# Kernel tuning notes

Hardware: AMD Instinct MI355X
Metric: run time of the kernel (lower is better)

The kernel has to match this reference:

```python
import jax, jax.numpy as jnp
import numpy as np

S, N, IN = 4096, 32, 4
H, IF, SF, OUT = 64, 8, 4, 2
N_PAIRS = N * (N - 1)


def setup_inputs() -> dict:
    key = jax.random.key(0)
    ks = jax.random.split(key, 12)
    f = jax.random.normal
    return {
        "inputs": f(ks[0], (S, N, IN), jnp.float32),
        "L1W": f(ks[1], (H, IN), jnp.float32) * 0.1,
        "L1b": f(ks[2], (H,), jnp.float32) * 0.1,
        "L2W": f(ks[3], (H, H), jnp.float32) * 0.1,
        "L2b": f(ks[4], (H,), jnp.float32) * 0.1,
        "I1W": f(ks[5], (H, H), jnp.float32) * 0.1,
        "I2W": f(ks[6], (IF, H), jnp.float32) * 0.1,
        "I3": f(ks[7], (N_PAIRS, OUT, IF // OUT), jnp.float32) * 0.01,
        "S1W": f(ks[8], (SF, IN), jnp.float32) * 0.1,
        "S1b": f(ks[9], (SF,), jnp.float32) * 0.1,
        "S2W": f(ks[10], (N, OUT, SF // OUT), jnp.float32) * 0.01,
        "S2b": jnp.zeros((N, OUT), jnp.float32),
    }


def reference(inputs, L1W, L1b, L2W, L2b, I1W, I2W, I3, S1W, S1b, S2W, S2b):
    seq_len, n_obj = inputs.shape[:2]
    out_size = S2b.shape[1]

    # shared encoders (torch Linear: x @ W.T + b)
    h = jax.nn.relu(inputs @ L1W.T + L1b)
    h = jax.nn.relu(h @ L2W.T + L2b)          # [S, N, H]
    hs = jax.nn.relu(inputs @ S1W.T + S1b)    # [S, N, SF]

    # all pairwise differences Xi - Xj -> edge MLP (no biases)
    diff = h[:, :, None, :] - h[:, None, :, :]      # [S, N, N, H]
    pair = jnp.tanh(diff @ I1W.T)                   # [S, N, N, H]
    pair = jnp.tanh(pair @ I2W.T)                   # [S, N, N, IF]
    k_int = pair.shape[-1] // out_size
    pair = pair.reshape(seq_len, n_obj, n_obj, out_size, k_int)

    # scatter per-pair weights I3 into dense [N, N, OUT, k] using the
    # row-major Table ordering (i, j != i); diagonal stays zero, which
    # matches the original since diag pairwise features are exactly 0.
    ii, jj = np.nonzero(~np.eye(n_obj, dtype=bool))
    I3d = jnp.zeros((n_obj, n_obj, out_size, k_int), I3.dtype).at[ii, jj].set(I3)

    interaction = jnp.einsum('sijdk,ijdk->sid', pair, I3d)  # [S, N, OUT]

    k_self = hs.shape[-1] // out_size
    hs = hs.reshape(seq_len, n_obj, out_size, k_self)
    self_term = jnp.einsum('sidk,idk->sid', hs, S2W) + S2b  # [S, N, OUT]

    return interaction + self_term
```

## Files before the change

kernel.cpp:

```cpp
#include <hip/hip_runtime.h>
#include <math.h>

#define SEQ   4096
#define NOBJ  32
#define IN_F  4
#define HID   64
#define IFEAT 8
#define NPAIR_HALF 496
#define NTILE 31

#define TWO_LOG2E 2.8853900817779268f

#if __has_builtin(__builtin_amdgcn_exp2f)
  #define EXP2F(x) __builtin_amdgcn_exp2f(x)
#else
  #define EXP2F(x) exp2f(x)
#endif

typedef _Float16 h2    __attribute__((ext_vector_type(2)));
typedef _Float16 f16x8 __attribute__((ext_vector_type(8)));
typedef float    f32x4 __attribute__((ext_vector_type(4)));

__device__ __forceinline__ h2 pack2(float a, float b) {
  return __builtin_bit_cast(h2, __builtin_amdgcn_cvt_pkrtz(a, b));
}
__device__ __forceinline__ unsigned pbits(h2 v) { return __builtin_bit_cast(unsigned, v); }

__device__ __forceinline__ f16x8 pack8(float4 a, float4 b) {
  int4 v;
  v.x = (int)pbits(pack2(a.x, a.y));
  v.y = (int)pbits(pack2(a.z, a.w));
  v.z = (int)pbits(pack2(b.x, b.y));
  v.w = (int)pbits(pack2(b.z, b.w));
  return __builtin_bit_cast(f16x8, v);
}

__device__ __forceinline__ f16x8 pack8f(const float* r) {
  int4 v;
  v.x = (int)pbits(pack2(r[0], r[1]));
  v.y = (int)pbits(pack2(r[2], r[3]));
  v.z = (int)pbits(pack2(r[4], r[5]));
  v.w = (int)pbits(pack2(r[6], r[7]));
  return __builtin_bit_cast(f16x8, v);
}

__device__ __forceinline__ float tanh_u(float x) {
  float e = EXP2F(x * TWO_LOG2E);
  float r = __builtin_amdgcn_rcpf(e + 1.0f);
  return fmaf(-2.0f, r, 1.0f);
}

__device__ __forceinline__ int pair_cum(int i) { return (i * (63 - i)) >> 1; }

__device__ __forceinline__ void pair_decode(int q, int& i, int& j) {
  int ii = (int)((63.0f - sqrtf(3969.0f - 8.0f * (float)q)) * 0.5f);
  if (ii > 0 && pair_cum(ii) > q) --ii;
  if (pair_cum(ii + 1) <= q)     ++ii;
  i = ii;
  j = ii + 1 + (q - pair_cum(ii));
}

__global__ __launch_bounds__(256, 4) void magnet_fused(
    const float* __restrict__ x,
    const float* __restrict__ L1W,
    const float* __restrict__ L1b,
    const float* __restrict__ L2W,
    const float* __restrict__ L2b,
    const float* __restrict__ I1W,
    const float* __restrict__ I2W,
    const float* __restrict__ I3,
    const float* __restrict__ S1W,
    const float* __restrict__ S1b,
    const float* __restrict__ S2W,
    const float* __restrict__ S2b,
    float* __restrict__ out)
{
  __shared__ __align__(16) float smem[4224];
  unsigned*       sAtp = (unsigned*)smem;
  unsigned*       sBtp = (unsigned*)smem;
  _Float16*       sv   = (_Float16*)smem;
  float*          sE   = smem + 1152;
  unsigned*       wB   = (unsigned*)(smem + 3328);
  float*          part = smem + 3328;
  float*          sx   = smem + 3840;
  float*          sW   = smem + 3968;
  unsigned short* ptab = (unsigned short*)(smem + 3976);

  const int t = threadIdx.x;
  const int s = blockIdx.x;

  if (t < NOBJ * IN_F) sx[t] = x[s * (NOBJ * IN_F) + t];
  if (t < IFEAT) {
    float a = 0.0f;
    const float4* w = (const float4*)(I2W + t * HID);
    #pragma unroll
    for (int c = 0; c < 16; ++c) { float4 v = w[c]; a += (v.x + v.y) + (v.z + v.w); }
    sW[t] = a;
  }
  #pragma unroll
  for (int idx = t; idx < 512; idx += 256) {
    const int n = idx >> 5, k2 = idx & 31;
    wB[idx] = (n < IFEAT)
      ? pbits(pack2(I2W[n * HID + 2 * k2], I2W[n * HID + 2 * k2 + 1])) : 0u;
  }
  #pragma unroll
  for (int q = t; q < NPAIR_HALF; q += 256) {
    int i, j; pair_decode(q, i, j);
    ptab[q] = (unsigned short)((i << 8) | j);
  }
  __syncthreads();

  {
    const int n = t & 31, gI = t >> 5, kb = gI * 8;
    const float x0 = sx[n * 4 + 0], x1 = sx[n * 4 + 1];
    const float x2 = sx[n * 4 + 2], x3 = sx[n * 4 + 3];
    float a[8];
    #pragma unroll
    for (int r = 0; r < 8; ++r) {
      const int k = kb + r;
      const float4 w = *(const float4*)(L1W + k * 4);
      float v = L1b[k];
      v = fmaf(x0, w.x, v); v = fmaf(x1, w.y, v);
      v = fmaf(x2, w.z, v); v = fmaf(x3, w.w, v);
      a[r] = fmaxf(v, 0.0f);
    }
    int4 pk;
    pk.x = (int)pbits(pack2(a[0], a[1]));
    pk.y = (int)pbits(pack2(a[2], a[3]));
    pk.z = (int)pbits(pack2(a[4], a[5]));
    pk.w = (int)pbits(pack2(a[6], a[7]));
    *(int4*)(sAtp + n * 36 + gI * 4) = pk;
  }
  __syncthreads();

  const int lane = t & 63;
  const int wv   = t >> 6;
  const int qd   = lane >> 4;
  const int ln   = lane & 15;

  {
    const int m = 16 * wv + ln;
    const float* wr = L2W + m * HID;
    const f16x8 A0 = pack8(*(const float4*)(wr + 8 * qd),
                           *(const float4*)(wr + 8 * qd + 4));
    const f16x8 A1 = pack8(*(const float4*)(wr + 32 + 8 * qd),
                           *(const float4*)(wr + 32 + 8 * qd + 4));
    const float4 bias = *(const float4*)(L2b + 16 * wv + 4 * qd);
    unsigned pk[4];
    #pragma unroll
    for (int nt = 0; nt < 2; ++nt) {
      const int n = nt * 16 + ln;
      const f16x8 B0 = __builtin_bit_cast(f16x8, *(const int4*)(sAtp + n * 36 + 4 * qd));
      const f16x8 B1 = __builtin_bit_cast(f16x8, *(const int4*)(sAtp + n * 36 + 16 + 4 * qd));
      f32x4 c; c[0] = bias.x; c[1] = bias.y; c[2] = bias.z; c[3] = bias.w;
      c = __builtin_amdgcn_mfma_f32_16x16x32_f16(A0, B0, c, 0, 0, 0);
      c = __builtin_amdgcn_mfma_f32_16x16x32_f16(A1, B1, c, 0, 0, 0);
      pk[nt * 2]     = pbits(pack2(fmaxf(c[0], 0.f), fmaxf(c[1], 0.f)));
      pk[nt * 2 + 1] = pbits(pack2(fmaxf(c[2], 0.f), fmaxf(c[3], 0.f)));
    }
    __syncthreads();
    #pragma unroll
    for (int nt = 0; nt < 2; ++nt) {
      const int n = nt * 16 + ln;
      sBtp[n * 36 + 8 * wv + 2 * qd]     = pk[nt * 2];
      sBtp[n * 36 + 8 * wv + 2 * qd + 1] = pk[nt * 2 + 1];
    }
  }
  __syncthreads();

  {
    const int m = 16 * wv + ln;
    const float* wr = I1W + m * HID;
    const f16x8 A0 = pack8(*(const float4*)(wr + 8 * qd),
                           *(const float4*)(wr + 8 * qd + 4));
    const f16x8 A1 = pack8(*(const float4*)(wr + 32 + 8 * qd),
                           *(const float4*)(wr + 32 + 8 * qd + 4));
    #pragma unroll
    for (int nt = 0; nt < 2; ++nt) {
      const int n = nt * 16 + ln;
      const f16x8 B0 = __builtin_bit_cast(f16x8, *(const int4*)(sBtp + n * 36 + 4 * qd));
      const f16x8 B1 = __builtin_bit_cast(f16x8, *(const int4*)(sBtp + n * 36 + 16 + 4 * qd));
      f32x4 c; c[0] = 0.f; c[1] = 0.f; c[2] = 0.f; c[3] = 0.f;
      c = __builtin_amdgcn_mfma_f32_16x16x32_f16(A0, B0, c, 0, 0, 0);
      c = __builtin_amdgcn_mfma_f32_16x16x32_f16(A1, B1, c, 0, 0, 0);
      #pragma unroll
      for (int r = 0; r < 4; ++r) {
        const int mo = 16 * wv + 4 * qd + r;
        float gp = fminf(fmaxf(c[r] * TWO_LOG2E, -60.0f), 60.0f);
        sE[n * 68 + mo] = EXP2F(gp);
      }
    }
  }
  __syncthreads();

  {
    const f16x8 B0 = __builtin_bit_cast(f16x8, *(const int4*)(wB + ln * 32 + 4 * qd));
    const f16x8 B1 = __builtin_bit_cast(f16x8, *(const int4*)(wB + ln * 32 + 16 + 4 * qd));
    const float Wf = sW[ln & 7];

    for (int tile = wv; tile < NTILE; tile += 4) {
      const unsigned pij = ptab[tile * 16 + ln];
      const int i = pij >> 8, j = pij & 255;
      const float* Ei = sE + i * 68 + qd * 8;
      const float* Ej = sE + j * 68 + qd * 8;
      const float4 e0 = *(const float4*)(Ei);
      const float4 e1 = *(const float4*)(Ei + 4);
      const float4 e2 = *(const float4*)(Ei + 32);
      const float4 e3 = *(const float4*)(Ei + 36);
      const float4 f0 = *(const float4*)(Ej);
      const float4 f1 = *(const float4*)(Ej + 4);
      const float4 f2 = *(const float4*)(Ej + 32);
      const float4 f3 = *(const float4*)(Ej + 36);
      float r0[8], r1[8];
      #pragma unroll
      for (int c = 0; c < 4; ++c) {
        r0[c]     = (&f0.x)[c] * __builtin_amdgcn_rcpf((&e0.x)[c] + (&f0.x)[c]);
        r0[4 + c] = (&f1.x)[c] * __builtin_amdgcn_rcpf((&e1.x)[c] + (&f1.x)[c]);
        r1[c]     = (&f2.x)[c] * __builtin_amdgcn_rcpf((&e2.x)[c] + (&f2.x)[c]);
        r1[4 + c] = (&f3.x)[c] * __builtin_amdgcn_rcpf((&e3.x)[c] + (&f3.x)[c]);
      }
      const f16x8 A0 = pack8f(r0);
      const f16x8 A1 = pack8f(r1);
      f32x4 c; c[0] = 0.f; c[1] = 0.f; c[2] = 0.f; c[3] = 0.f;
      c = __builtin_amdgcn_mfma_f32_16x16x32_f16(A0, B0, c, 0, 0, 0);
      c = __builtin_amdgcn_mfma_f32_16x16x32_f16(A1, B1, c, 0, 0, 0);
      if (ln < IFEAT) {
        #pragma unroll
        for (int r = 0; r < 4; ++r) {
          const float v = tanh_u(fmaf(-2.0f, c[r], Wf));
          sv[(tile * 16 + 4 * qd + r) * 8 + ln] = (_Float16)v;
        }
      }
    }
  }
  __syncthreads();

  {
    const int i = t >> 3, d = (t >> 2) & 1, qtr = t & 3;
    const int mend = (qtr == 3) ? 31 : (qtr * 8 + 8);
    float sum = 0.0f;
    for (int m = qtr * 8; m < mend; ++m) {
      const int j = m + (m >= i);
      int q; float sgn;
      if (j > i) { q = pair_cum(i) + (j - i - 1); sgn =  1.0f; }
      else       { q = pair_cum(j) + (i - j - 1); sgn = -1.0f; }
      const h2* vp = (const h2*)(sv + q * 8 + d * 4);
      const h2 va = vp[0], vb = vp[1];
      const float4 cf = *(const float4*)(I3 + (i * 31 + m) * 8 + d * 4);
      float dot;
      dot = cf.x * (float)va.x;
      dot = fmaf(cf.y, (float)va.y, dot);
      dot = fmaf(cf.z, (float)vb.x, dot);
      dot = fmaf(cf.w, (float)vb.y, dot);
      sum = fmaf(sgn, dot, sum);
    }
    part[t] = sum;
  }
  __syncthreads();

  if (t < 64) {
    const int i = t >> 1, d = t & 1;
    float sum = part[t * 4] + part[t * 4 + 1] + part[t * 4 + 2] + part[t * 4 + 3];

    float res = S2b[t] + sum;
    #pragma unroll
    for (int k = 0; k < 2; ++k) {
      const int f = d * 2 + k;
      float hs = S1b[f];
      hs = fmaf(sx[i * 4 + 0], S1W[f * 4 + 0], hs);
      hs = fmaf(sx[i * 4 + 1], S1W[f * 4 + 1], hs);
      hs = fmaf(sx[i * 4 + 2], S1W[f * 4 + 2], hs);
      hs = fmaf(sx[i * 4 + 3], S1W[f * 4 + 3], hs);
      hs = fmaxf(hs, 0.0f);
      res = fmaf(hs, S2W[i * 4 + d * 2 + k], res);
    }
    out[s * (NOBJ * 2) + t] = res;
  }
}

extern "C" void kernel_launch(void* const* d_in, const int* in_sizes, int n_in,
                              void* d_out, int out_size, void* d_ws, size_t ws_size,
                              hipStream_t stream) {
  const float* x   = (const float*)d_in[0];
  const float* L1W = (const float*)d_in[1];
  const float* L1b = (const float*)d_in[2];
  const float* L2W = (const float*)d_in[3];
  const float* L2b = (const float*)d_in[4];
  const float* I1W = (const float*)d_in[5];
  const float* I2W = (const float*)d_in[6];
  const float* I3  = (const float*)d_in[7];
  const float* S1W = (const float*)d_in[8];
  const float* S1b = (const float*)d_in[9];
  const float* S2W = (const float*)d_in[10];
  const float* S2b = (const float*)d_in[11];
  float* outp = (float*)d_out;

  magnet_fused<<<SEQ, 256, 0, stream>>>(x, L1W, L1b, L2W, L2b, I1W, I2W, I3,
                                        S1W, S1b, S2W, S2b, outp);
}
```

Baseline: 119.2 us.

## Process two sequence steps per block to amortize weight loads and setup

Each block now handles two sequence positions instead of one, halving the grid. Weight fragments (L2W, I1W, I2W packs), pair tables and per-block setup are loaded once and reused for both samples. Shared memory grows from about 17KB to about 39KB, which may cut occupancy, and there are fewer blocks to spread across CUs. The I2W row-sum is also parallelized across 64 threads.

Result: no change. 117.9 us (-1.1%).

```diff
diff --git a/kernel.cpp b/kernel.cpp
--- a/kernel.cpp
+++ b/kernel.cpp
@@ -75,27 +75,24 @@
     const float* __restrict__ S2b,
     float* __restrict__ out)
 {
-  __shared__ __align__(16) float smem[4224];
-  unsigned*       sAtp = (unsigned*)smem;
-  unsigned*       sBtp = (unsigned*)smem;
-  _Float16*       sv   = (_Float16*)smem;
-  float*          sE   = smem + 1152;
-  unsigned*       wB   = (unsigned*)(smem + 3328);
-  float*          part = smem + 3328;
-  float*          sx   = smem + 3840;
-  float*          sW   = smem + 3968;
-  unsigned short* ptab = (unsigned short*)(smem + 3976);
-
-  const int t = threadIdx.x;
-  const int s = blockIdx.x;
-
-  if (t < NOBJ * IN_F) sx[t] = x[s * (NOBJ * IN_F) + t];
-  if (t < IFEAT) {
-    float a = 0.0f;
-    const float4* w = (const float4*)(I2W + t * HID);
-    #pragma unroll
-    for (int c = 0; c < 16; ++c) { float4 v = w[c]; a += (v.x + v.y) + (v.z + v.w); }
-    sW[t] = a;
+  __shared__ __align__(16) float smem[9728];
+  float*          sE0  = smem + 2304;
+  unsigned*       wB   = (unsigned*)(smem + 8640);
+  float*          part = smem + 8640;
+  float*          sx   = smem + 9152;
+  float*          sW   = smem + 9408;
+  unsigned short* ptab = (unsigned short*)(smem + 9416);
+  float*          swpart = smem + 9664;
+
+  const int t  = threadIdx.x;
+  const int s0 = blockIdx.x * 2;
+
+  sx[t] = x[s0 * 128 + t];
+  if (t < 64) {
+    const int f = t >> 3, seg = t & 7;
+    const float4 a = *(const float4*)(I2W + f * HID + seg * 8);
+    const float4 b = *(const float4*)(I2W + f * HID + seg * 8 + 4);
+    swpart[t] = ((a.x + a.y) + (a.z + a.w)) + ((b.x + b.y) + (b.z + b.w));
   }
   #pragma unroll
   for (int idx = t; idx < 512; idx += 256) {
@@ -109,27 +106,40 @@
     ptab[q] = (unsigned short)((i << 8) | j);
   }
   __syncthreads();
+  if (t < IFEAT) {
+    float a = 0.0f;
+    #pragma unroll
+    for (int c = 0; c < 8; ++c) a += swpart[t * 8 + c];
+    sW[t] = a;
+  }
 
   {
     const int n = t & 31, gI = t >> 5, kb = gI * 8;
-    const float x0 = sx[n * 4 + 0], x1 = sx[n * 4 + 1];
-    const float x2 = sx[n * 4 + 2], x3 = sx[n * 4 + 3];
-    float a[8];
+    float a[2][8];
     #pragma unroll
     for (int r = 0; r < 8; ++r) {
       const int k = kb + r;
       const float4 w = *(const float4*)(L1W + k * 4);
-      float v = L1b[k];
-      v = fmaf(x0, w.x, v); v = fmaf(x1, w.y, v);
-      v = fmaf(x2, w.z, v); v = fmaf(x3, w.w, v);
-      a[r] = fmaxf(v, 0.0f);
-    }
-    int4 pk;
-    pk.x = (int)pbits(pack2(a[0], a[1]));
-    pk.y = (int)pbits(pack2(a[2], a[3]));
-    pk.z = (int)pbits(pack2(a[4], a[5]));
-    pk.w = (int)pbits(pack2(a[6], a[7]));
-    *(int4*)(sAtp + n * 36 + gI * 4) = pk;
+      const float bias = L1b[k];
+      #pragma unroll
+      for (int ss = 0; ss < 2; ++ss) {
+        const float* xv = sx + ss * 128 + n * 4;
+        float v = bias;
+        v = fmaf(xv[0], w.x, v); v = fmaf(xv[1], w.y, v);
+        v = fmaf(xv[2], w.z, v); v = fmaf(xv[3], w.w, v);
+        a[ss][r] = fmaxf(v, 0.0f);
+      }
+    }
+    #pragma unroll
+    for (int ss = 0; ss < 2; ++ss) {
+      unsigned* sAtp = (unsigned*)(smem + ss * 1152);
+      int4 pk;
+      pk.x = (int)pbits(pack2(a[ss][0], a[ss][1]));
+      pk.y = (int)pbits(pack2(a[ss][2], a[ss][3]));
+      pk.z = (int)pbits(pack2(a[ss][4], a[ss][5]));
+      pk.w = (int)pbits(pack2(a[ss][6], a[ss][7]));
+      *(int4*)(sAtp + n * 36 + gI * 4) = pk;
+    }
   }
   __syncthreads();
 
@@ -146,24 +156,32 @@
     const f16x8 A1 = pack8(*(const float4*)(wr + 32 + 8 * qd),
                            *(const float4*)(wr + 32 + 8 * qd + 4));
     const float4 bias = *(const float4*)(L2b + 16 * wv + 4 * qd);
-    unsigned pk[4];
-    #pragma unroll
-    for (int nt = 0; nt < 2; ++nt) {
-      const int n = nt * 16 + ln;
-      const f16x8 B0 = __builtin_bit_cast(f16x8, *(const int4*)(sAtp + n * 36 + 4 * qd));
-      const f16x8 B1 = __builtin_bit_cast(f16x8, *(const int4*)(sAtp + n * 36 + 16 + 4 * qd));
-      f32x4 c; c[0] = bias.x; c[1] = bias.y; c[2] = bias.z; c[3] = bias.w;
-      c = __builtin_amdgcn_mfma_f32_16x16x32_f16(A0, B0, c, 0, 0, 0);
-      c = __builtin_amdgcn_mfma_f32_16x16x32_f16(A1, B1, c, 0, 0, 0);
-      pk[nt * 2]     = pbits(pack2(fmaxf(c[0], 0.f), fmaxf(c[1], 0.f)));
-      pk[nt * 2 + 1] = pbits(pack2(fmaxf(c[2], 0.f), fmaxf(c[3], 0.f)));
+    unsigned pk[2][4];
+    #pragma unroll
+    for (int ss = 0; ss < 2; ++ss) {
+      const unsigned* sAtp = (const unsigned*)(smem + ss * 1152);
+      #pragma unroll
+      for (int nt = 0; nt < 2; ++nt) {
+        const int n = nt * 16 + ln;
+        const f16x8 B0 = __builtin_bit_cast(f16x8, *(const int4*)(sAtp + n * 36 + 4 * qd));
+        const f16x8 B1 = __builtin_bit_cast(f16x8, *(const int4*)(sAtp + n * 36 + 16 + 4 * qd));
+        f32x4 c; c[0] = bias.x; c[1] = bias.y; c[2] = bias.z; c[3] = bias.w;
+        c = __builtin_amdgcn_mfma_f32_16x16x32_f16(A0, B0, c, 0, 0, 0);
+        c = __builtin_amdgcn_mfma_f32_16x16x32_f16(A1, B1, c, 0, 0, 0);
+        pk[ss][nt * 2]     = pbits(pack2(fmaxf(c[0], 0.f), fmaxf(c[1], 0.f)));
+        pk[ss][nt * 2 + 1] = pbits(pack2(fmaxf(c[2], 0.f), fmaxf(c[3], 0.f)));
+      }
     }
     __syncthreads();
     #pragma unroll
-    for (int nt = 0; nt < 2; ++nt) {
-      const int n = nt * 16 + ln;
-      sBtp[n * 36 + 8 * wv + 2 * qd]     = pk[nt * 2];
-      sBtp[n * 36 + 8 * wv + 2 * qd + 1] = pk[nt * 2 + 1];
+    for (int ss = 0; ss < 2; ++ss) {
+      unsigned* sBtp = (unsigned*)(smem + ss * 1152);
+      #pragma unroll
+      for (int nt = 0; nt < 2; ++nt) {
+        const int n = nt * 16 + ln;
+        sBtp[n * 36 + 8 * wv + 2 * qd]     = pk[ss][nt * 2];
+        sBtp[n * 36 + 8 * wv + 2 * qd + 1] = pk[ss][nt * 2 + 1];
+      }
     }
   }
   __syncthreads();
@@ -176,18 +194,23 @@
     const f16x8 A1 = pack8(*(const float4*)(wr + 32 + 8 * qd),
                            *(const float4*)(wr + 32 + 8 * qd + 4));
     #pragma unroll
-    for (int nt = 0; nt < 2; ++nt) {
-      const int n = nt * 16 + ln;
-      const f16x8 B0 = __builtin_bit_cast(f16x8, *(const int4*)(sBtp + n * 36 + 4 * qd));
-      const f16x8 B1 = __builtin_bit_cast(f16x8, *(const int4*)(sBtp + n * 36 + 16 + 4 * qd));
-      f32x4 c; c[0] = 0.f; c[1] = 0.f; c[2] = 0.f; c[3] = 0.f;
-      c = __builtin_amdgcn_mfma_f32_16x16x32_f16(A0, B0, c, 0, 0, 0);
-      c = __builtin_amdgcn_mfma_f32_16x16x32_f16(A1, B1, c, 0, 0, 0);
-      #pragma unroll
-      for (int r = 0; r < 4; ++r) {
-        const int mo = 16 * wv + 4 * qd + r;
-        float gp = fminf(fmaxf(c[r] * TWO_LOG2E, -60.0f), 60.0f);
-        sE[n * 68 + mo] = EXP2F(gp);
+    for (int ss = 0; ss < 2; ++ss) {
+      const unsigned* sBtp = (const unsigned*)(smem + ss * 1152);
+      float* sE = sE0 + ss * 2176;
+      #pragma unroll
+      for (int nt = 0; nt < 2; ++nt) {
+        const int n = nt * 16 + ln;
+        const f16x8 B0 = __builtin_bit_cast(f16x8, *(const int4*)(sBtp + n * 36 + 4 * qd));
+        const f16x8 B1 = __builtin_bit_cast(f16x8, *(const int4*)(sBtp + n * 36 + 16 + 4 * qd));
+        f32x4 c; c[0] = 0.f; c[1] = 0.f; c[2] = 0.f; c[3] = 0.f;
+        c = __builtin_amdgcn_mfma_f32_16x16x32_f16(A0, B0, c, 0, 0, 0);
+        c = __builtin_amdgcn_mfma_f32_16x16x32_f16(A1, B1, c, 0, 0, 0);
+        #pragma unroll
+        for (int r = 0; r < 4; ++r) {
+          const int mo = 16 * wv + 4 * qd + r;
+          float gp = fminf(fmaxf(c[r] * TWO_LOG2E, -60.0f), 60.0f);
+          sE[n * 68 + mo] = EXP2F(gp);
+        }
       }
     }
   }
@@ -201,45 +224,52 @@
     for (int tile = wv; tile < NTILE; tile += 4) {
       const unsigned pij = ptab[tile * 16 + ln];
       const int i = pij >> 8, j = pij & 255;
-      const float* Ei = sE + i * 68 + qd * 8;
-      const float* Ej = sE + j * 68 + qd * 8;
-      const float4 e0 = *(const float4*)(Ei);
-      const float4 e1 = *(const float4*)(Ei + 4);
-      const float4 e2 = *(const float4*)(Ei + 32);
-      const float4 e3 = *(const float4*)(Ei + 36);
-      const float4 f0 = *(const float4*)(Ej);
-      const float4 f1 = *(const float4*)(Ej + 4);
-      const float4 f2 = *(const float4*)(Ej + 32);
-      const float4 f3 = *(const float4*)(Ej + 36);
-      float r0[8], r1[8];
-      #pragma unroll
-      for (int c = 0; c < 4; ++c) {
-        r0[c]     = (&f0.x)[c] * __builtin_amdgcn_rcpf((&e0.x)[c] + (&f0.x)[c]);
-        r0[4 + c] = (&f1.x)[c] * __builtin_amdgcn_rcpf((&e1.x)[c] + (&f1.x)[c]);
-        r1[c]     = (&f2.x)[c] * __builtin_amdgcn_rcpf((&e2.x)[c] + (&f2.x)[c]);
-        r1[4 + c] = (&f3.x)[c] * __builtin_amdgcn_rcpf((&e3.x)[c] + (&f3.x)[c]);
-      }
-      const f16x8 A0 = pack8f(r0);
-      const f16x8 A1 = pack8f(r1);
-      f32x4 c; c[0] = 0.f; c[1] = 0.f; c[2] = 0.f; c[3] = 0.f;
-      c = __builtin_amdgcn_mfma_f32_16x16x32_f16(A0, B0, c, 0, 0, 0);
-      c = __builtin_amdgcn_mfma_f32_16x16x32_f16(A1, B1, c, 0, 0, 0);
-      if (ln < IFEAT) {
+      #pragma unroll
+      for (int ss = 0; ss < 2; ++ss) {
+        const float* sE = sE0 + ss * 2176;
+        _Float16* sv = ss ? (_Float16*)(smem + 6656) : (_Float16*)smem;
+        const float* Ei = sE + i * 68 + qd * 8;
+        const float* Ej = sE + j * 68 + qd * 8;
+        const float4 e0 = *(const float4*)(Ei);
+        const float4 e1 = *(const float4*)(Ei + 4);
+        const float4 e2 = *(const float4*)(Ei + 32);
+        const float4 e3 = *(const float4*)(Ei + 36);
+        const float4 f0 = *(const float4*)(Ej);
+        const float4 f1 = *(const float4*)(Ej + 4);
+        const float4 f2 = *(const float4*)(Ej + 32);
+        const float4 f3 = *(const float4*)(Ej + 36);
+        float r0[8], r1[8];
         #pragma unroll
-        for (int r = 0; r < 4; ++r) {
-          const float v = tanh_u(fmaf(-2.0f, c[r], Wf));
-          sv[(tile * 16 + 4 * qd + r) * 8 + ln] = (_Float16)v;
+        for (int c = 0; c < 4; ++c) {
+          r0[c]     = (&f0.x)[c] * __builtin_amdgcn_rcpf((&e0.x)[c] + (&f0.x)[c]);
+          r0[4 + c] = (&f1.x)[c] * __builtin_amdgcn_rcpf((&e1.x)[c] + (&f1.x)[c]);
+          r1[c]     = (&f2.x)[c] * __builtin_amdgcn_rcpf((&e2.x)[c] + (&f2.x)[c]);
+          r1[4 + c] = (&f3.x)[c] * __builtin_amdgcn_rcpf((&e3.x)[c] + (&f3.x)[c]);
         }
-      }
-    }
-  }
-  __syncthreads();
-
-  {
-    const int i = t >> 3, d = (t >> 2) & 1, qtr = t & 3;
-    const int mend = (qtr == 3) ? 31 : (qtr * 8 + 8);
+        const f16x8 A0 = pack8f(r0);
+        const f16x8 A1 = pack8f(r1);
+        f32x4 c; c[0] = 0.f; c[1] = 0.f; c[2] = 0.f; c[3] = 0.f;
+        c = __builtin_amdgcn_mfma_f32_16x16x32_f16(A0, B0, c, 0, 0, 0);
+        c = __builtin_amdgcn_mfma_f32_16x16x32_f16(A1, B1, c, 0, 0, 0);
+        if (ln < IFEAT) {
+          #pragma unroll
+          for (int r = 0; r < 4; ++r) {
+            const float v = tanh_u(fmaf(-2.0f, c[r], Wf));
+            sv[(tile * 16 + 4 * qd + r) * 8 + ln] = (_Float16)v;
+          }
+        }
+      }
+    }
+  }
+  __syncthreads();
+
+  {
+    const int ss = t >> 7, i = (t >> 2) & 31, d = (t >> 1) & 1, half = t & 1;
+    const _Float16* sv = ss ? (const _Float16*)(smem + 6656) : (const _Float16*)smem;
+    const int msta = half * 16;
+    const int mend = half ? 31 : 16;
     float sum = 0.0f;
-    for (int m = qtr * 8; m < mend; ++m) {
+    for (int m = msta; m < mend; ++m) {
       const int j = m + (m >= i);
       int q; float sgn;
       if (j > i) { q = pair_cum(i) + (j - i - 1); sgn =  1.0f; }
@@ -258,23 +288,25 @@
   }
   __syncthreads();
 
-  if (t < 64) {
-    const int i = t >> 1, d = t & 1;
-    float sum = part[t * 4] + part[t * 4 + 1] + part[t * 4 + 2] + part[t * 4 + 3];
-
-    float res = S2b[t] + sum;
+  if (t < 128) {
+    const int ss = t >> 6, i = (t >> 1) & 31, d = t & 1;
+    const int pbase = ss * 128 + i * 4 + d * 2;
+    float sum = part[pbase] + part[pbase + 1];
+
+    float res = S2b[i * 2 + d] + sum;
+    const float* xv = sx + ss * 128 + i * 4;
     #pragma unroll
     for (int k = 0; k < 2; ++k) {
       const int f = d * 2 + k;
       float hs = S1b[f];
-      hs = fmaf(sx[i * 4 + 0], S1W[f * 4 + 0], hs);
-      hs = fmaf(sx[i * 4 + 1], S1W[f * 4 + 1], hs);
-      hs = fmaf(sx[i * 4 + 2], S1W[f * 4 + 2], hs);
-      hs = fmaf(sx[i * 4 + 3], S1W[f * 4 + 3], hs);
+      hs = fmaf(xv[0], S1W[f * 4 + 0], hs);
+      hs = fmaf(xv[1], S1W[f * 4 + 1], hs);
+      hs = fmaf(xv[2], S1W[f * 4 + 2], hs);
+      hs = fmaf(xv[3], S1W[f * 4 + 3], hs);
       hs = fmaxf(hs, 0.0f);
       res = fmaf(hs, S2W[i * 4 + d * 2 + k], res);
     }
-    out[s * (NOBJ * 2) + t] = res;
+    out[(s0 + ss) * (NOBJ * 2) + i * 2 + d] = res;
   }
 }
 
@@ -295,6 +327,6 @@
   const float* S2b = (const float*)d_in[11];
   float* outp = (float*)d_out;
 
-  magnet_fused<<<SEQ, 256, 0, stream>>>(x, L1W, L1b, L2W, L2b, I1W, I2W, I3,
-                                        S1W, S1b, S2W, S2b, outp);
-}
+  magnet_fused<<<SEQ / 2, 256, 0, stream>>>(x, L1W, L1b, L2W, L2b, I1W, I2W, I3,
+                                            S1W, S1b, S2W, S2b, outp);
+}
```
